# Performance work log

Measured on AMD Instinct MI355X. Metric: run time of the kernel, lower is better.

Reference implementation:

```python
import jax, jax.numpy as jnp
import numpy as np

N_VARS = 32        # n_variables
TEMPERATURE = 1.0  # softmax temperature (default)


def setup_inputs() -> dict:
    key = jax.random.key(0)
    k1, k2 = jax.random.split(key)
    B, C, T = 16, 3072, 2048  # C = n_var * (hidden_dim + n_var) = 32*(64+32)
    x = jax.random.normal(k1, (B, C, T), dtype=jnp.float32)
    x_instant = jax.random.normal(k2, (B, C, T), dtype=jnp.float32)
    return {"x": x, "x_instant": x_instant}


def _split_context_attention(v, n):
    B, _, T = v.shape
    v = v.reshape(B, n, -1, T)          # (B, n, hidden+n, T)
    attn = v[:, :, :n, :]               # (B, n, n, T) attention logits
    ctx = v[:, :, n:, :]                # (B, n, hidden, T)
    return ctx, attn


def reference(x, x_instant):
    n = N_VARS
    B, _, T = x.shape
    ctx, attn = _split_context_attention(x, n)
    ctx_i, attn_i = _split_context_attention(x_instant, n)
    ctx = jnp.concatenate([ctx, ctx_i], axis=-3)     # (B, 2n, hidden, T)
    attn = jnp.concatenate([attn, attn_i], axis=-2)  # (B, n, 2n, T)
    attn = jax.nn.softmax(attn / TEMPERATURE, axis=-2)
    # aggregate contexts with attention weights
    out = jnp.einsum('bijt,bjdt->bidt', attn, ctx)   # (B, n, hidden, T)
    out = out.reshape(B, -1, T)                      # (B, n*hidden, T)
    # ConvertInstant: zero the instantaneous self-edge (j = n + i), then sum chunks
    a1 = attn[:, :, :n, :]
    a2 = attn[:, :, n:, :]
    diag = jnp.eye(n, dtype=bool)[None, :, :, None]  # (1, n, n, 1)
    a2 = jnp.where(diag, jnp.zeros((), dtype=attn.dtype), a2)
    attentions = a1 + a2                             # (B, n, n, T)
    return out, attentions
```

## Files before the change

kernel.cpp:

```cpp
#include <hip/hip_runtime.h>


typedef unsigned int uint_t;

constexpr int Bq = 16, Cq = 3072, Tq = 2048;
constexpr int TT = 32;
constexpr int TILES = Tq / TT;
constexpr int NBLK = Bq * TILES;
constexpr size_t ATT_OFF = (size_t)Bq * 2048 * Tq;

__global__ __launch_bounds__(1024, 4) void attn_v5(const float* __restrict__ x,
                                                   const float* __restrict__ xi,
                                                   float* __restrict__ out)
{
    __shared__ uint_t plds[32 * 32 * 32];

    const int b    = (int)blockIdx.x >> 6;
    const int tile = (int)blockIdx.x & (TILES - 1);
    const int t0   = tile * TT;
    const int tl   = (int)threadIdx.x & 31;
    const int slot = (int)threadIdx.x >> 5;
    const int xw   = (tl & 7) << 2;

    const float* xb  = x  + (size_t)b * Cq * Tq + t0 + tl;
    const float* xib = xi + (size_t)b * Cq * Tq + t0 + tl;

    {
        const int i = slot;
        float p[64];
#pragma unroll
        for (int j = 0; j < 32; ++j) p[j]      = xb [(size_t)(i * 96 + j) * Tq];
#pragma unroll
        for (int j = 0; j < 32; ++j) p[j + 32] = xib[(size_t)(i * 96 + j) * Tq];
        float m = p[0];
#pragma unroll
        for (int j = 1; j < 64; ++j) m = fmaxf(m, p[j]);
        float s = 0.f;
#pragma unroll
        for (int j = 0; j < 64; ++j) { p[j] = __expf(p[j] - m); s += p[j]; }
        const float inv = 1.f / s;
#pragma unroll
        for (int j = 0; j < 64; ++j) p[j] *= inv;

        float* ao = out + ATT_OFF + ((size_t)(b * 32 + i) * 32) * Tq + t0 + tl;
#pragma unroll
        for (int j = 0; j < 32; ++j) {
            float v = p[j] + ((j == i) ? 0.f : p[j + 32]);
            __builtin_nontemporal_store(v, &ao[(size_t)j * Tq]);
        }
#pragma unroll
        for (int k = 0; k < 32; ++k) {
            uint_t b0 = __float_as_uint(p[2 * k]);
            uint_t b1 = __float_as_uint(p[2 * k + 1]);
            uint_t lo = (b0 + 0x7fffu + ((b0 >> 16) & 1u)) >> 16;
            uint_t hi = (b1 + 0x7fffu + ((b1 >> 16) & 1u)) >> 16;
            plds[k * 1024 + tl * 32 + (i ^ xw)] = lo | (hi << 16);
        }
    }
    __syncthreads();

    const int ig = slot & 3;
    const int dg = slot >> 2;
    const int d0 = dg * 8;
    const int pbase = tl * 32;

    const float* cx  = x  + (size_t)b * Cq * Tq + (size_t)(32 + d0) * Tq + t0 + tl;
    const float* cxi = xi + (size_t)b * Cq * Tq + (size_t)(32 + d0) * Tq + t0 + tl;

    float acc[8][8];
#pragma unroll
    for (int r = 0; r < 8; ++r)
#pragma unroll
        for (int dd = 0; dd < 8; ++dd) acc[r][dd] = 0.f;

#pragma unroll 2
    for (int k = 0; k < 32; ++k) {
        const float* base = (k < 16) ? cx : cxi;
        const int kg = k & 15;
        const uint4 wa = *reinterpret_cast<const uint4*>(
            &plds[k * 1024 + pbase + ((ig * 8 + 0) ^ xw)]);
        const uint4 wb = *reinterpret_cast<const uint4*>(
            &plds[k * 1024 + pbase + ((ig * 8 + 4) ^ xw)]);
        float pj0[8], pj1[8];
        pj0[0] = __uint_as_float(wa.x << 16);  pj1[0] = __uint_as_float(wa.x & 0xffff0000u);
        pj0[1] = __uint_as_float(wa.y << 16);  pj1[1] = __uint_as_float(wa.y & 0xffff0000u);
        pj0[2] = __uint_as_float(wa.z << 16);  pj1[2] = __uint_as_float(wa.z & 0xffff0000u);
        pj0[3] = __uint_as_float(wa.w << 16);  pj1[3] = __uint_as_float(wa.w & 0xffff0000u);
        pj0[4] = __uint_as_float(wb.x << 16);  pj1[4] = __uint_as_float(wb.x & 0xffff0000u);
        pj0[5] = __uint_as_float(wb.y << 16);  pj1[5] = __uint_as_float(wb.y & 0xffff0000u);
        pj0[6] = __uint_as_float(wb.z << 16);  pj1[6] = __uint_as_float(wb.z & 0xffff0000u);
        pj0[7] = __uint_as_float(wb.w << 16);  pj1[7] = __uint_as_float(wb.w & 0xffff0000u);

        float c0[8], c1[8];
#pragma unroll
        for (int dd = 0; dd < 8; ++dd)
            c0[dd] = base[(size_t)(kg * 192 + dd) * Tq];
#pragma unroll
        for (int dd = 0; dd < 8; ++dd)
            c1[dd] = base[(size_t)(kg * 192 + 96 + dd) * Tq];

#pragma unroll
        for (int r = 0; r < 8; ++r)
#pragma unroll
            for (int dd = 0; dd < 8; ++dd)
                acc[r][dd] += pj0[r] * c0[dd] + pj1[r] * c1[dd];
    }

    float* ob = out + (size_t)b * 2048 * Tq + t0 + tl;
#pragma unroll
    for (int r = 0; r < 8; ++r)
#pragma unroll
        for (int dd = 0; dd < 8; ++dd) {
            int ch = (ig * 8 + r) * 64 + d0 + dd;
            __builtin_nontemporal_store(acc[r][dd], &ob[(size_t)ch * Tq]);
        }
}

extern "C" void kernel_launch(void* const* d_in, const int* in_sizes, int n_in,
                              void* d_out, int out_size, void* d_ws, size_t ws_size,
                              hipStream_t stream) {
    const float* x  = (const float*)d_in[0];
    const float* xi = (const float*)d_in[1];
    float* out = (float*)d_out;
    attn_v5<<<dim3(NBLK), dim3(1024), 0, stream>>>(x, xi, out);
}
```

Measured before the change: 308.0 us.

## Compute attention-weighted context aggregation with bf16 MFMA via LDS-staged tiles

New measurement: 270.8 us. -12.1%, faster.

```diff
diff --git a/kernel.cpp b/kernel.cpp
--- a/kernel.cpp
+++ b/kernel.cpp
@@ -1,30 +1,37 @@
 #include <hip/hip_runtime.h>
+#include <stdint.h>
 
 
 typedef unsigned int uint_t;
+typedef float  f32x4   __attribute__((ext_vector_type(4)));
+typedef short  short8v __attribute__((ext_vector_type(8)));
 
 constexpr int Bq = 16, Cq = 3072, Tq = 2048;
-constexpr int TT = 32;
-constexpr int TILES = Tq / TT;
-constexpr int NBLK = Bq * TILES;
+constexpr int TT = 32, TILES = 64, NBLK = Bq * TILES;
 constexpr size_t ATT_OFF = (size_t)Bq * 2048 * Tq;
+constexpr int TBS = 4224;
+constexpr int LDS_BYTES = 135168;
 
-__global__ __launch_bounds__(1024, 4) void attn_v5(const float* __restrict__ x,
-                                                   const float* __restrict__ xi,
-                                                   float* __restrict__ out)
+__global__ __launch_bounds__(1024, 1) void attn_v12(const float* __restrict__ x,
+                                                    const float* __restrict__ xi,
+                                                    float* __restrict__ out)
 {
-    __shared__ uint_t plds[32 * 32 * 32];
+    __shared__ __align__(16) unsigned char smem[LDS_BYTES];
+    unsigned short* LU = (unsigned short*)smem;
+    uint_t*         LW = (uint_t*)smem;
+    float*          LF = (float*)smem;
 
+    const int tid  = (int)threadIdx.x;
     const int b    = (int)blockIdx.x >> 6;
     const int tile = (int)blockIdx.x & (TILES - 1);
     const int t0   = tile * TT;
-    const int tl   = (int)threadIdx.x & 31;
-    const int slot = (int)threadIdx.x >> 5;
-    const int xw   = (tl & 7) << 2;
+    const int tl   = tid & 31;
+    const int slot = tid >> 5;
 
     const float* xb  = x  + (size_t)b * Cq * Tq + t0 + tl;
     const float* xib = xi + (size_t)b * Cq * Tq + t0 + tl;
 
+    uint_t pk[32];
     {
         const int i = slot;
         float p[64];
@@ -54,66 +61,94 @@
             uint_t b1 = __float_as_uint(p[2 * k + 1]);
             uint_t lo = (b0 + 0x7fffu + ((b0 >> 16) & 1u)) >> 16;
             uint_t hi = (b1 + 0x7fffu + ((b1 >> 16) & 1u)) >> 16;
-            plds[k * 1024 + tl * 32 + (i ^ xw)] = lo | (hi << 16);
+            pk[k] = lo | (hi << 16);
         }
     }
-    __syncthreads();
 
-    const int ig = slot & 3;
-    const int dg = slot >> 2;
-    const int d0 = dg * 8;
-    const int pbase = tl * 32;
+    const int fw  = ((slot >> 2) & 3) ^ (slot & 3);
+    const int TBw = tl * TBS + (tl & 7) * 16;
 
-    const float* cx  = x  + (size_t)b * Cq * Tq + (size_t)(32 + d0) * Tq + t0 + tl;
-    const float* cxi = xi + (size_t)b * Cq * Tq + (size_t)(32 + d0) * Tq + t0 + tl;
-
-    float acc[8][8];
-#pragma unroll
-    for (int r = 0; r < 8; ++r)
-#pragma unroll
-        for (int dd = 0; dd < 8; ++dd) acc[r][dd] = 0.f;
-
-#pragma unroll 2
-    for (int k = 0; k < 32; ++k) {
-        const float* base = (k < 16) ? cx : cxi;
-        const int kg = k & 15;
-        const uint4 wa = *reinterpret_cast<const uint4*>(
-            &plds[k * 1024 + pbase + ((ig * 8 + 0) ^ xw)]);
-        const uint4 wb = *reinterpret_cast<const uint4*>(
-            &plds[k * 1024 + pbase + ((ig * 8 + 4) ^ xw)]);
-        float pj0[8], pj1[8];
-        pj0[0] = __uint_as_float(wa.x << 16);  pj1[0] = __uint_as_float(wa.x & 0xffff0000u);
-        pj0[1] = __uint_as_float(wa.y << 16);  pj1[1] = __uint_as_float(wa.y & 0xffff0000u);
-        pj0[2] = __uint_as_float(wa.z << 16);  pj1[2] = __uint_as_float(wa.z & 0xffff0000u);
-        pj0[3] = __uint_as_float(wa.w << 16);  pj1[3] = __uint_as_float(wa.w & 0xffff0000u);
-        pj0[4] = __uint_as_float(wb.x << 16);  pj1[4] = __uint_as_float(wb.x & 0xffff0000u);
-        pj0[5] = __uint_as_float(wb.y << 16);  pj1[5] = __uint_as_float(wb.y & 0xffff0000u);
-        pj0[6] = __uint_as_float(wb.z << 16);  pj1[6] = __uint_as_float(wb.z & 0xffff0000u);
-        pj0[7] = __uint_as_float(wb.w << 16);  pj1[7] = __uint_as_float(wb.w & 0xffff0000u);
-
-        float c0[8], c1[8];
-#pragma unroll
-        for (int dd = 0; dd < 8; ++dd)
-            c0[dd] = base[(size_t)(kg * 192 + dd) * Tq];
-#pragma unroll
-        for (int dd = 0; dd < 8; ++dd)
-            c1[dd] = base[(size_t)(kg * 192 + 96 + dd) * Tq];
+    const int l   = tid & 63;
+    const int wv  = tid >> 6;
+    const int frd = ((l >> 2) & 3) ^ (l & 3);
+    const int kbr = (((l >> 4) ^ frd) & 3) * 16;
+    const int rA  = (l & 15) * 64;
 
 #pragma unroll
-        for (int r = 0; r < 8; ++r)
+    for (int dh = 0; dh < 2; ++dh) {
+        f32x4 acc[2][2][2];
 #pragma unroll
-            for (int dd = 0; dd < 8; ++dd)
-                acc[r][dd] += pj0[r] * c0[dd] + pj1[r] * c1[dd];
+        for (int q = 0; q < 2; ++q)
+#pragma unroll
+            for (int s = 0; s < 2; ++s)
+#pragma unroll
+                for (int dt = 0; dt < 2; ++dt) acc[q][s][dt] = (f32x4)(0.f);
+
+#pragma unroll
+        for (int jh = 0; jh < 2; ++jh) {
+#pragma unroll
+            for (int m = 0; m < 16; ++m) {
+                const int kbx  = (m >> 2) ^ fw;
+                const int byte = TBw + slot * 64 + kbx * 16 + ((2 * m) & 7) * 2;
+                LW[byte >> 2] = pk[jh * 16 + m];
+            }
+            {
+                const float* src = (jh == 0) ? x : xi;
+                const float* sp  = src + (size_t)b * Cq * Tq
+                                 + (size_t)(32 + dh * 32 + slot) * Tq + t0 + tl;
+#pragma unroll 8
+                for (int kk = 0; kk < 32; ++kk) {
+                    const float v = sp[(size_t)kk * 96 * Tq];
+                    const uint_t bb = __float_as_uint(v);
+                    const unsigned short h =
+                        (unsigned short)((bb + 0x7fffu + ((bb >> 16) & 1u)) >> 16);
+                    const int kbx  = (kk >> 3) ^ fw;
+                    const int byte = TBw + 2048 + slot * 64 + kbx * 16 + (kk & 7) * 2;
+                    LU[byte >> 1] = h;
+                }
+            }
+            __syncthreads();
+
+#pragma unroll
+            for (int q = 0; q < 2; ++q) {
+                const int tloc = 2 * wv + q;
+                const int base = tloc * TBS + (tloc & 7) * 16;
+                const short8v A0 = *(const short8v*)(smem + base        + rA + kbr);
+                const short8v A1 = *(const short8v*)(smem + base + 1024 + rA + kbr);
+                const short8v B0 = *(const short8v*)(smem + base + 2048 + rA + kbr);
+                const short8v B1 = *(const short8v*)(smem + base + 3072 + rA + kbr);
+                acc[q][0][0] = __builtin_amdgcn_mfma_f32_16x16x32_bf16(A0, B0, acc[q][0][0], 0, 0, 0);
+                acc[q][0][1] = __builtin_amdgcn_mfma_f32_16x16x32_bf16(A0, B1, acc[q][0][1], 0, 0, 0);
+                acc[q][1][0] = __builtin_amdgcn_mfma_f32_16x16x32_bf16(A1, B0, acc[q][1][0], 0, 0, 0);
+                acc[q][1][1] = __builtin_amdgcn_mfma_f32_16x16x32_bf16(A1, B1, acc[q][1][1], 0, 0, 0);
+            }
+            __syncthreads();
+        }
+
+#pragma unroll
+        for (int q = 0; q < 2; ++q)
+#pragma unroll
+            for (int s = 0; s < 2; ++s)
+#pragma unroll
+                for (int dt = 0; dt < 2; ++dt)
+#pragma unroll
+                    for (int ri = 0; ri < 4; ++ri) {
+                        const int ii = s * 16 + (l >> 4) * 4 + ri;
+                        const int dl = dt * 16 + (l & 15);
+                        LF[(ii * 32 + dl) * 33 + 2 * wv + q] = acc[q][s][dt][ri];
+                    }
+        __syncthreads();
+        {
+            float* ob = out + (size_t)b * 2048 * Tq + t0 + tl;
+#pragma unroll 8
+            for (int kk = 0; kk < 32; ++kk) {
+                const int ch = kk * 64 + dh * 32 + slot;
+                __builtin_nontemporal_store(LF[(kk * 32 + slot) * 33 + tl],
+                                            &ob[(size_t)ch * Tq]);
+            }
+        }
+        __syncthreads();
     }
-
-    float* ob = out + (size_t)b * 2048 * Tq + t0 + tl;
-#pragma unroll
-    for (int r = 0; r < 8; ++r)
-#pragma unroll
-        for (int dd = 0; dd < 8; ++dd) {
-            int ch = (ig * 8 + r) * 64 + d0 + dd;
-            __builtin_nontemporal_store(acc[r][dd], &ob[(size_t)ch * Tq]);
-        }
 }
 
 extern "C" void kernel_launch(void* const* d_in, const int* in_sizes, int n_in,
@@ -122,5 +157,5 @@
     const float* x  = (const float*)d_in[0];
     const float* xi = (const float*)d_in[1];
     float* out = (float*)d_out;
-    attn_v5<<<dim3(NBLK), dim3(1024), 0, stream>>>(x, xi, out);
+    attn_v12<<<dim3(NBLK), dim3(1024), 0, stream>>>(x, xi, out);
 }
```
